# Optimization experiments

Measured on AMD Instinct MI355X. Metric: run time of the kernel, lower is better.

The kernel has to match this reference:

```python
import jax, jax.numpy as jnp
import numpy as np

N_NODES = 100000
N_EDGES = 1600000
DIM = 128
NUM_CLASSES = 40


def setup_inputs() -> dict:
    key = jax.random.key(0)
    ks = jax.random.split(key, 8)
    scale = 1.0 / np.sqrt(DIM)
    return {
        "node_embeddings": jax.random.normal(ks[0], (N_NODES, DIM), jnp.float32),
        "edge_index": jax.random.randint(ks[1], (N_EDGES, 2), 0, N_NODES, jnp.int32),
        "W1a": jax.random.normal(ks[2], (DIM, DIM), jnp.float32) * scale,
        "b1a": jnp.zeros((DIM,), jnp.float32),
        "W1b": jax.random.normal(ks[3], (DIM, DIM), jnp.float32) * scale,
        "b1b": jnp.zeros((DIM,), jnp.float32),
        "W2a": jax.random.normal(ks[4], (DIM, NUM_CLASSES), jnp.float32) * scale,
        "b2a": jnp.zeros((NUM_CLASSES,), jnp.float32),
        "W2b": jax.random.normal(ks[5], (NUM_CLASSES, NUM_CLASSES), jnp.float32) * (1.0 / np.sqrt(NUM_CLASSES)),
        "b2b": jnp.zeros((NUM_CLASSES,), jnp.float32),
    }


def _gin_conv(x, src, dst, Wa, ba, Wb, bb, n_nodes):
    # GIN aggregation with eps=0: h_i = (1+eps)*x_i + sum_{j in N(i)} x_j
    agg = jax.ops.segment_sum(x[src], dst, num_segments=n_nodes)
    h = agg + x
    # nn: Dense -> ReLU -> Dense
    h = jax.nn.relu(h @ Wa + ba)
    return h @ Wb + bb


def reference(node_embeddings, edge_index, W1a, b1a, W1b, b1b, W2a, b2a, W2b, b2b):
    src = edge_index[:, 0]
    dst = edge_index[:, 1]
    n = node_embeddings.shape[0]
    # dropout layers are identity at inference (predict: training=False)
    x = jax.nn.relu(_gin_conv(node_embeddings, src, dst, W1a, b1a, W1b, b1b, n))
    x = _gin_conv(x, src, dst, W2a, b2a, W2b, b2b, n)
    return jax.nn.softmax(x, axis=-1)
```

## Files before the change

kernel.cpp:

```cpp
#include <hip/hip_runtime.h>
#include <hip/hip_fp16.h>

#define N_NODES 100000
#define N_EDGES 1600000
#define DIM 128
#define NC 40

#define BUCKET_SHIFT 7
#define BUCKET_NODES 128
#define NBUCKET ((N_NODES + BUCKET_NODES - 1) / BUCKET_NODES)
#define SEGCAP 3072
#define NBIN 1024
#define EPB 4096
#define NBLK_FILL ((N_EDGES + EPB - 1) / EPB)

#define NBLK_CVT (N_NODES * DIM / 8 / 256)
#define NBLK_PACK 20

typedef _Float16 f16x8 __attribute__((ext_vector_type(8)));
typedef float f32x4 __attribute__((ext_vector_type(4)));

__device__ __forceinline__ void acc_row8(float* acc, uint4 v) {
    __half2 h;
    float2 f;
    *(unsigned*)&h = v.x; f = __half22float2(h); acc[0] += f.x; acc[1] += f.y;
    *(unsigned*)&h = v.y; f = __half22float2(h); acc[2] += f.x; acc[3] += f.y;
    *(unsigned*)&h = v.z; f = __half22float2(h); acc[4] += f.x; acc[5] += f.y;
    *(unsigned*)&h = v.w; f = __half22float2(h); acc[6] += f.x; acc[7] += f.y;
}

__global__ __launch_bounds__(256) void k_cvt_pack(const float* __restrict__ x, __half* __restrict__ xh,
                                                  __half* __restrict__ y,
                                                  const float* __restrict__ W1a, const float* __restrict__ W1b,
                                                  const float* __restrict__ W2a, const float* __restrict__ W2b,
                                                  _Float16* __restrict__ Pa, _Float16* __restrict__ Pb,
                                                  _Float16* __restrict__ Pc, float4* __restrict__ Wq) {
    int b = blockIdx.x, tid = threadIdx.x;
    if (b >= NBLK_CVT) {
        int bid = b - NBLK_CVT;
        if (bid < 16) {
            const float* W = (bid < 8) ? W1a : W1b;
            _Float16* P = (bid < 8) ? Pa : Pb;
            int t = (bid & 7) * 256 + tid;
            int l = t & 63, nt = (t >> 6) & 7, kt = t >> 9;
            int n = nt * 16 + (l & 15);
            int kb = kt * 32 + (l >> 4) * 8;
            #pragma unroll
            for (int j = 0; j < 8; ++j)
                P[(size_t)t * 8 + j] = (_Float16)W[(size_t)(kb + j) * DIM + n];
        } else if (bid < 19) {
            int t = (bid - 16) * 256 + tid;
            if (t < 768) {
                int l = t & 63, u = t >> 6;
                int nt = u % 3, kt = u / 3;
                int n = nt * 16 + (l & 15);
                int kb = kt * 32 + (l >> 4) * 8;
                #pragma unroll
                for (int j = 0; j < 8; ++j) {
                    float wv = (n < NC) ? W2a[(size_t)(kb + j) * NC + n] : 0.f;
                    Pc[(size_t)t * 8 + j] = (_Float16)wv;
                }
            }
        } else {
            for (int u = tid; u < 10 * NC; u += 256) {
                int q = u / NC, c = u - q * NC;
                float4 wv;
                wv.x = W2b[(4 * q + 0) * NC + c];
                wv.y = W2b[(4 * q + 1) * NC + c];
                wv.z = W2b[(4 * q + 2) * NC + c];
                wv.w = W2b[(4 * q + 3) * NC + c];
                Wq[u] = wv;
            }
        }
        return;
    }

    int i = b * 256 + tid;
    if (b == 0) {
        if (tid < 16) ((uint4*)xh)[(size_t)N_NODES * (DIM / 8) + tid] = (uint4){0, 0, 0, 0};
        else if (tid < 21) ((uint4*)y)[(size_t)N_NODES * 5 + tid - 16] = (uint4){0, 0, 0, 0};
    }
    float4 v0 = ((const float4*)x)[(size_t)i * 2];
    float4 v1 = ((const float4*)x)[(size_t)i * 2 + 1];
    __half2 h01 = __float22half2_rn(make_float2(v0.x, v0.y));
    __half2 h23 = __float22half2_rn(make_float2(v0.z, v0.w));
    __half2 h45 = __float22half2_rn(make_float2(v1.x, v1.y));
    __half2 h67 = __float22half2_rn(make_float2(v1.z, v1.w));
    uint4 o;
    o.x = *(unsigned*)&h01; o.y = *(unsigned*)&h23;
    o.z = *(unsigned*)&h45; o.w = *(unsigned*)&h67;
    ((uint4*)xh)[i] = o;
}

__global__ __launch_bounds__(256) void k_binfill(const int2* __restrict__ ei, int* __restrict__ cnt,
                                                 int* __restrict__ seg) {
    __shared__ int hist[NBIN];
    __shared__ int offs[NBIN];
    __shared__ int gbase[NBIN];
    __shared__ int lcnt[NBIN];
    __shared__ int lds[EPB];
    __shared__ short binof[EPB];
    __shared__ int wt[4];
    int t = threadIdx.x;
    int e0 = blockIdx.x * EPB;
    int bec = N_EDGES - e0; if (bec > EPB) bec = EPB;

    int2 er[EPB / 256];
    #pragma unroll
    for (int k = 0; k < EPB / 256; ++k) {
        int i = e0 + t + k * 256;
        er[k] = (i < N_EDGES) ? ei[i] : (int2){0, -1};
    }

    #pragma unroll
    for (int j = 0; j < NBIN / 256; ++j) { hist[t + j * 256] = 0; lcnt[t + j * 256] = 0; }
    __syncthreads();

    #pragma unroll
    for (int k = 0; k < EPB / 256; ++k)
        if (er[k].y >= 0) atomicAdd(&hist[er[k].y >> BUCKET_SHIFT], 1);
    __syncthreads();

    int lane = t & 63, w = t >> 6;
    int h[4], p = 0;
    #pragma unroll
    for (int j = 0; j < 4; ++j) { h[j] = hist[t * 4 + j]; p += h[j]; }
    int inc = p;
    #pragma unroll
    for (int d = 1; d < 64; d <<= 1) {
        int u = __shfl_up(inc, d, 64);
        if (lane >= d) inc += u;
    }
    if (lane == 63) wt[w] = inc;
    __syncthreads();
    int add = inc - p;
    for (int k = 0; k < w; ++k) add += wt[k];
    int run = add;
    #pragma unroll
    for (int j = 0; j < 4; ++j) { offs[t * 4 + j] = run; run += h[j]; }
    __syncthreads();

    #pragma unroll
    for (int j = 0; j < 4; ++j) {
        int b = t * 4 + j;
        if (b < NBUCKET && h[j] > 0) gbase[b] = b * SEGCAP + atomicAdd(&cnt[b], h[j]);
    }
    __syncthreads();

    #pragma unroll
    for (int k = 0; k < EPB / 256; ++k) {
        if (er[k].y >= 0) {
            int b = er[k].y >> BUCKET_SHIFT;
            int pos = offs[b] + atomicAdd(&lcnt[b], 1);
            lds[pos] = er[k].x | ((er[k].y & (BUCKET_NODES - 1)) << 17);
            binof[pos] = (short)b;
        }
    }
    __syncthreads();

    for (int i = t; i < bec; i += 256) {
        int lo = binof[i];
        seg[gbase[lo] + (i - offs[lo])] = lds[i];
    }
}

__global__ __launch_bounds__(256) void k_csr_local(int* __restrict__ dg, const int* __restrict__ cnt,
                                                   const int* __restrict__ seg, int* __restrict__ rs,
                                                   int* __restrict__ csr) {
    __shared__ int ldg[BUCKET_NODES];
    __shared__ int cur[BUCKET_NODES];
    __shared__ int wq0;
    int t = threadIdx.x, b = blockIdx.x;
    int n0 = b * BUCKET_NODES;
    int nn = N_NODES - n0; if (nn > BUCKET_NODES) nn = BUCKET_NODES;
    if (t < BUCKET_NODES) ldg[t] = 0;
    __syncthreads();

    int c = cnt[b];
    for (int i = t; i < c; i += 256)
        atomicAdd(&ldg[(seg[b * SEGCAP + i] >> 17) & (BUCKET_NODES - 1)], 1);
    __syncthreads();

    int d = (t < BUCKET_NODES) ? ldg[t] : 0;
    int lane = t & 63, w2 = t >> 6;
    int incl = d;
    #pragma unroll
    for (int s = 1; s < 64; s <<= 1) {
        int u = __shfl_up(incl, s, 64);
        if (lane >= s) incl += u;
    }
    if (w2 == 0 && lane == 63) wq0 = incl;
    __syncthreads();
    int excl = incl - d + ((w2 == 1) ? wq0 : 0);
    if (t < nn) {
        int base = b * SEGCAP + excl;
        cur[t] = base;
        rs[n0 + t] = base;
        dg[n0 + t] = d;
    }
    __syncthreads();

    for (int i = t; i < c; i += 256) {
        int e = seg[b * SEGCAP + i];
        int dl = (e >> 17) & (BUCKET_NODES - 1);
        int pos = atomicAdd(&cur[dl], 1);
        csr[pos] = e & 0x1FFFF;
    }
}

__global__ __launch_bounds__(256) void k_gather1(const __half* __restrict__ xh, const int* __restrict__ rs,
                                                 const int* __restrict__ dg, const int* __restrict__ csr_src,
                                                 __half* __restrict__ hp) {
    int l = threadIdx.x & 63, wid = threadIdx.x >> 6;
    int n = __builtin_amdgcn_readfirstlane(blockIdx.x * 4 + wid);
    int grp = l >> 4, q = l & 15;
    const uint4* x4 = (const uint4*)xh;

    uint4 sv;
    if (grp == 0) sv = x4[(size_t)n * 16 + q];

    float acc[8] = {0.f, 0.f, 0.f, 0.f, 0.f, 0.f, 0.f, 0.f};
    int i0 = rs[n], e = i0 + dg[n];
    int niter = (e - i0 + 7) >> 3;
    uint4 cur[2];
    if (niter > 0) {
        #pragma unroll
        for (int u = 0; u < 2; ++u) {
            int idx = i0 + u * 4 + grp;
            int s = (idx < e) ? csr_src[idx] : N_NODES;
            cur[u] = x4[(size_t)s * 16 + q];
        }
    }
    for (int k = 1; k < niter; ++k) {
        int base = i0 + k * 8;
        uint4 nxt[2];
        #pragma unroll
        for (int u = 0; u < 2; ++u) {
            int idx = base + u * 4 + grp;
            int s = (idx < e) ? csr_src[idx] : N_NODES;
            nxt[u] = x4[(size_t)s * 16 + q];
        }
        acc_row8(acc, cur[0]); cur[0] = nxt[0];
        acc_row8(acc, cur[1]); cur[1] = nxt[1];
    }
    if (niter > 0) {
        acc_row8(acc, cur[0]);
        acc_row8(acc, cur[1]);
    }
    #pragma unroll
    for (int k2 = 0; k2 < 8; ++k2) {
        acc[k2] += __shfl_xor(acc[k2], 16);
        acc[k2] += __shfl_xor(acc[k2], 32);
    }

    if (grp == 0) {
        acc_row8(acc, sv);
        __half2 o0 = __float22half2_rn(make_float2(acc[0], acc[1]));
        __half2 o1 = __float22half2_rn(make_float2(acc[2], acc[3]));
        __half2 o2 = __float22half2_rn(make_float2(acc[4], acc[5]));
        __half2 o3 = __float22half2_rn(make_float2(acc[6], acc[7]));
        uint4 ov;
        ov.x = *(unsigned*)&o0; ov.y = *(unsigned*)&o1;
        ov.z = *(unsigned*)&o2; ov.w = *(unsigned*)&o3;
        ((uint4*)hp)[(size_t)n * 16 + q] = ov;
    }
}

__global__ __launch_bounds__(256) void k_mlp(const __half* __restrict__ hp,
    const _Float16* __restrict__ Pa, const _Float16* __restrict__ Pb, const _Float16* __restrict__ Pc,
    const float* __restrict__ b1a, const float* __restrict__ b1b, __half* __restrict__ y) {
    __shared__ _Float16 A[64][136];
    __shared__ _Float16 H[64][136];
    int t = threadIdx.x;
    size_t row0 = (size_t)blockIdx.x * 64;

    for (int i = t; i < 1024; i += 256) {
        int r = i >> 4, c = i & 15;
        size_t g = row0 + r;
        if (g >= N_NODES) g = N_NODES - 1;
        uint4 v = ((const uint4*)(hp + g * DIM))[c];
        *(uint4*)&A[r][c * 8] = v;
    }
    __syncthreads();

    int w = t >> 6, l = t & 63;
    int lrow = l & 15;
    int kq = (l >> 4) * 8;
    int csub = (l >> 4) * 4;
    int ccol = l & 15;
    int nt0 = 2 * w, nt1 = 2 * w + 1;

    {
        f16x8 bf0[4], bf1[4];
        #pragma unroll
        for (int kt = 0; kt < 4; ++kt) {
            bf0[kt] = *(const f16x8*)(Pa + ((size_t)((kt << 3) + nt0) * 64 + l) * 8);
            bf1[kt] = *(const f16x8*)(Pa + ((size_t)((kt << 3) + nt1) * 64 + l) * 8);
        }
        float b0 = b1a[nt0 * 16 + ccol], b1 = b1a[nt1 * 16 + ccol];
        #pragma unroll
        for (int rt = 0; rt < 4; ++rt) {
            f16x8 af[4];
            #pragma unroll
            for (int kt = 0; kt < 4; ++kt) af[kt] = *(const f16x8*)&A[rt * 16 + lrow][kt * 32 + kq];
            f32x4 a0 = (f32x4){b0, b0, b0, b0}, a1 = (f32x4){b1, b1, b1, b1};
            #pragma unroll
            for (int kt = 0; kt < 4; ++kt) {
                a0 = __builtin_amdgcn_mfma_f32_16x16x32_f16(af[kt], bf0[kt], a0, 0, 0, 0);
                a1 = __builtin_amdgcn_mfma_f32_16x16x32_f16(af[kt], bf1[kt], a1, 0, 0, 0);
            }
            #pragma unroll
            for (int r = 0; r < 4; ++r) {
                H[rt * 16 + csub + r][nt0 * 16 + ccol] = (_Float16)fmaxf(a0[r], 0.f);
                H[rt * 16 + csub + r][nt1 * 16 + ccol] = (_Float16)fmaxf(a1[r], 0.f);
            }
        }
    }
    __syncthreads();

    {
        f16x8 bf0[4], bf1[4];
        #pragma unroll
        for (int kt = 0; kt < 4; ++kt) {
            bf0[kt] = *(const f16x8*)(Pb + ((size_t)((kt << 3) + nt0) * 64 + l) * 8);
            bf1[kt] = *(const f16x8*)(Pb + ((size_t)((kt << 3) + nt1) * 64 + l) * 8);
        }
        float b0 = b1b[nt0 * 16 + ccol], b1 = b1b[nt1 * 16 + ccol];
        #pragma unroll
        for (int rt = 0; rt < 4; ++rt) {
            f16x8 af[4];
            #pragma unroll
            for (int kt = 0; kt < 4; ++kt) af[kt] = *(const f16x8*)&H[rt * 16 + lrow][kt * 32 + kq];
            f32x4 a0 = (f32x4){b0, b0, b0, b0}, a1 = (f32x4){b1, b1, b1, b1};
            #pragma unroll
            for (int kt = 0; kt < 4; ++kt) {
                a0 = __builtin_amdgcn_mfma_f32_16x16x32_f16(af[kt], bf0[kt], a0, 0, 0, 0);
                a1 = __builtin_amdgcn_mfma_f32_16x16x32_f16(af[kt], bf1[kt], a1, 0, 0, 0);
            }
            #pragma unroll
            for (int r = 0; r < 4; ++r) {
                A[rt * 16 + csub + r][nt0 * 16 + ccol] = (_Float16)fmaxf(a0[r], 0.f);
                A[rt * 16 + csub + r][nt1 * 16 + ccol] = (_Float16)fmaxf(a1[r], 0.f);
            }
        }
    }
    __syncthreads();

    #pragma unroll
    for (int it = 0; it < 3; ++it) {
        int tt = w + 4 * it;
        int nt = tt % 3, rt = tt / 3;
        f16x8 bf[4], af[4];
        #pragma unroll
        for (int kt = 0; kt < 4; ++kt) {
            bf[kt] = *(const f16x8*)(Pc + ((size_t)(kt * 3 + nt) * 64 + l) * 8);
            af[kt] = *(const f16x8*)&A[rt * 16 + lrow][kt * 32 + kq];
        }
        f32x4 ya = (f32x4){0.f, 0.f, 0.f, 0.f};
        #pragma unroll
        for (int kt = 0; kt < 4; ++kt)
            ya = __builtin_amdgcn_mfma_f32_16x16x32_f16(af[kt], bf[kt], ya, 0, 0, 0);
        int col = nt * 16 + ccol;
        if (col < NC) {
            #pragma unroll
            for (int r = 0; r < 4; ++r) {
                size_t gr = row0 + rt * 16 + csub + r;
                if (gr < N_NODES) y[gr * NC + col] = __float2half(ya[r]);
            }
        }
    }
}

__global__ __launch_bounds__(256) void k_gather2(const __half* __restrict__ y, const int* __restrict__ rs,
                                                 const int* __restrict__ dg, const int* __restrict__ csr_src,
                                                 const float* __restrict__ b2a, const float4* __restrict__ Wq,
                                                 const float* __restrict__ b2b, float* __restrict__ out) {
    __shared__ float h2s[4][NC];
    int l = threadIdx.x & 63, wid = threadIdx.x >> 6;
    int n = __builtin_amdgcn_readfirstlane(blockIdx.x * 4 + wid);
    int g = l / 5, j = l - g * 5;
    const uint4* y4 = (const uint4*)y;

    float acc[8] = {0.f, 0.f, 0.f, 0.f, 0.f, 0.f, 0.f, 0.f};
    uint4 self;
    if (l < 5) self = y4[(size_t)n * 5 + j];

    int i0 = rs[n], d = dg[n];
    int e = i0 + d;
    uint4 c0, c1;
    {
        int iA = i0 + g;
        int sA = (g < 12 && iA < e) ? csr_src[iA] : N_NODES;
        c0 = y4[(size_t)sA * 5 + j];
        int iB = i0 + 12 + g;
        int sB = (g < 12 && iB < e) ? csr_src[iB] : N_NODES;
        c1 = y4[(size_t)sB * 5 + j];
    }
    int niter = (d + 23) / 24;
    for (int k = 1; k < niter; ++k) {
        int base = i0 + k * 24;
        int iA = base + g;
        int sA = (g < 12 && iA < e) ? csr_src[iA] : N_NODES;
        uint4 n0 = y4[(size_t)sA * 5 + j];
        int iB = base + 12 + g;
        int sB = (g < 12 && iB < e) ? csr_src[iB] : N_NODES;
        uint4 n1 = y4[(size_t)sB * 5 + j];
        acc_row8(acc, c0); c0 = n0;
        acc_row8(acc, c1); c1 = n1;
    }
    if (d > 0) {
        acc_row8(acc, c0);
        acc_row8(acc, c1);
    }
    if (l < 5) acc_row8(acc, self);

    #pragma unroll
    for (int k = 0; k < 8; ++k) acc[k] += __shfl_down(acc[k], 30);
    #pragma unroll
    for (int k = 0; k < 8; ++k) acc[k] += __shfl_down(acc[k], 15);
    #pragma unroll
    for (int k = 0; k < 8; ++k) acc[k] += __shfl_down(acc[k], 5) + __shfl_down(acc[k], 10);

    if (l < 5) {
        float4 b0 = *(const float4*)(b2a + 8 * l);
        float4 b1 = *(const float4*)(b2a + 8 * l + 4);
        float4 h0, h1;
        h0.x = fmaxf(acc[0] + b0.x, 0.f); h0.y = fmaxf(acc[1] + b0.y, 0.f);
        h0.z = fmaxf(acc[2] + b0.z, 0.f); h0.w = fmaxf(acc[3] + b0.w, 0.f);
        h1.x = fmaxf(acc[4] + b1.x, 0.f); h1.y = fmaxf(acc[5] + b1.y, 0.f);
        h1.z = fmaxf(acc[6] + b1.z, 0.f); h1.w = fmaxf(acc[7] + b1.w, 0.f);
        *(float4*)&h2s[wid][8 * l] = h0;
        *(float4*)&h2s[wid][8 * l + 4] = h1;
    }
    __threadfence_block();

    float logit = -__builtin_inff();
    if (l < NC) {
        float4 a4 = {0.f, 0.f, 0.f, 0.f};
        #pragma unroll
        for (int q = 0; q < 10; ++q) {
            float4 h4 = *(const float4*)&h2s[wid][4 * q];
            float4 w4 = Wq[q * NC + l];
            a4.x = fmaf(h4.x, w4.x, a4.x);
            a4.y = fmaf(h4.y, w4.y, a4.y);
            a4.z = fmaf(h4.z, w4.z, a4.z);
            a4.w = fmaf(h4.w, w4.w, a4.w);
        }
        logit = (a4.x + a4.y) + (a4.z + a4.w) + b2b[l];
    }
    float m = logit;
    #pragma unroll
    for (int d2 = 32; d2 >= 1; d2 >>= 1) m = fmaxf(m, __shfl_xor(m, d2, 64));
    float ev = (l < NC) ? __expf(logit - m) : 0.f;
    float s = ev;
    #pragma unroll
    for (int d2 = 32; d2 >= 1; d2 >>= 1) s += __shfl_xor(s, d2, 64);
    if (l < NC) out[(size_t)n * NC + l] = ev / s;
}

extern "C" void kernel_launch(void* const* d_in, const int* in_sizes, int n_in,
                              void* d_out, int out_size, void* d_ws, size_t ws_size,
                              hipStream_t stream) {
    const float* x   = (const float*)d_in[0];
    const int2*  ei  = (const int2*)d_in[1];
    const float* W1a = (const float*)d_in[2];
    const float* b1a = (const float*)d_in[3];
    const float* W1b = (const float*)d_in[4];
    const float* b1b = (const float*)d_in[5];
    const float* W2a = (const float*)d_in[6];
    const float* b2a = (const float*)d_in[7];
    const float* W2b = (const float*)d_in[8];
    const float* b2b = (const float*)d_in[9];
    float* out = (float*)d_out;

    char* w = (char*)d_ws;
    int*    dg     = (int*)(w + 0);
    int*    cnt    = (int*)(w + 400000);
    int*    rs     = (int*)(w + 403200);
    int*    csr    = (int*)(w + 803200);
    __half* xh     = (__half*)(w + 10412416);
    __half* hp     = (__half*)(w + 36012672);
    __half* y      = (__half*)(w + 61612672);
    _Float16* Pa   = (_Float16*)(w + 69612800);
    _Float16* Pb   = (_Float16*)(w + 69645568);
    _Float16* Pc   = (_Float16*)(w + 69678336);
    float4*   Wq   = (float4*)(w + 69690624);
    int*    seg    = (int*)hp;

    (void)hipMemsetAsync(w + 400000, 0, 3200, stream);
    k_cvt_pack <<<NBLK_CVT + NBLK_PACK, 256, 0, stream>>>(x, xh, y,
                                                          W1a, W1b, W2a, W2b, Pa, Pb, Pc, Wq);
    k_binfill  <<<NBLK_FILL, 256, 0, stream>>>(ei, cnt, seg);
    k_csr_local<<<NBUCKET, 256, 0, stream>>>(dg, cnt, seg, rs, csr);
    k_gather1  <<<N_NODES / 4, 256, 0, stream>>>(xh, rs, dg, csr, hp);
    k_mlp      <<<(N_NODES + 63) / 64, 256, 0, stream>>>(hp, Pa, Pb, Pc, b1a, b1b, y);
    k_gather2  <<<N_NODES / 4, 256, 0, stream>>>(y, rs, dg, csr, b2a, Wq, b2b, out);
}
```

Baseline: 300.7 us.

## Merge conversion/packing into CSR kernel and use LDS atomics for gather2 reduction

The fp32-to-fp16 conversion and weight packing move out of their own launch and into the CSR-building kernel as extra blocks, which removes one kernel launch and lets the two independent jobs run concurrently. In gather2, the shuffle-based cross-lane reduction and bias/ReLU step are replaced by float atomicAdds into a bias-initialised shared row, followed by an in-place ReLU. The atomics may contend on the same LDS addresses and make the summation order nondeterministic. The ordering between the bias write and the atomics relies only on __threadfence_block within a wave.

```diff
diff --git a/kernel.cpp b/kernel.cpp
--- a/kernel.cpp
+++ b/kernel.cpp
@@ -27,69 +27,6 @@
     *(unsigned*)&h = v.y; f = __half22float2(h); acc[2] += f.x; acc[3] += f.y;
     *(unsigned*)&h = v.z; f = __half22float2(h); acc[4] += f.x; acc[5] += f.y;
     *(unsigned*)&h = v.w; f = __half22float2(h); acc[6] += f.x; acc[7] += f.y;
-}
-
-__global__ __launch_bounds__(256) void k_cvt_pack(const float* __restrict__ x, __half* __restrict__ xh,
-                                                  __half* __restrict__ y,
-                                                  const float* __restrict__ W1a, const float* __restrict__ W1b,
-                                                  const float* __restrict__ W2a, const float* __restrict__ W2b,
-                                                  _Float16* __restrict__ Pa, _Float16* __restrict__ Pb,
-                                                  _Float16* __restrict__ Pc, float4* __restrict__ Wq) {
-    int b = blockIdx.x, tid = threadIdx.x;
-    if (b >= NBLK_CVT) {
-        int bid = b - NBLK_CVT;
-        if (bid < 16) {
-            const float* W = (bid < 8) ? W1a : W1b;
-            _Float16* P = (bid < 8) ? Pa : Pb;
-            int t = (bid & 7) * 256 + tid;
-            int l = t & 63, nt = (t >> 6) & 7, kt = t >> 9;
-            int n = nt * 16 + (l & 15);
-            int kb = kt * 32 + (l >> 4) * 8;
-            #pragma unroll
-            for (int j = 0; j < 8; ++j)
-                P[(size_t)t * 8 + j] = (_Float16)W[(size_t)(kb + j) * DIM + n];
-        } else if (bid < 19) {
-            int t = (bid - 16) * 256 + tid;
-            if (t < 768) {
-                int l = t & 63, u = t >> 6;
-                int nt = u % 3, kt = u / 3;
-                int n = nt * 16 + (l & 15);
-                int kb = kt * 32 + (l >> 4) * 8;
-                #pragma unroll
-                for (int j = 0; j < 8; ++j) {
-                    float wv = (n < NC) ? W2a[(size_t)(kb + j) * NC + n] : 0.f;
-                    Pc[(size_t)t * 8 + j] = (_Float16)wv;
-                }
-            }
-        } else {
-            for (int u = tid; u < 10 * NC; u += 256) {
-                int q = u / NC, c = u - q * NC;
-                float4 wv;
-                wv.x = W2b[(4 * q + 0) * NC + c];
-                wv.y = W2b[(4 * q + 1) * NC + c];
-                wv.z = W2b[(4 * q + 2) * NC + c];
-                wv.w = W2b[(4 * q + 3) * NC + c];
-                Wq[u] = wv;
-            }
-        }
-        return;
-    }
-
-    int i = b * 256 + tid;
-    if (b == 0) {
-        if (tid < 16) ((uint4*)xh)[(size_t)N_NODES * (DIM / 8) + tid] = (uint4){0, 0, 0, 0};
-        else if (tid < 21) ((uint4*)y)[(size_t)N_NODES * 5 + tid - 16] = (uint4){0, 0, 0, 0};
-    }
-    float4 v0 = ((const float4*)x)[(size_t)i * 2];
-    float4 v1 = ((const float4*)x)[(size_t)i * 2 + 1];
-    __half2 h01 = __float22half2_rn(make_float2(v0.x, v0.y));
-    __half2 h23 = __float22half2_rn(make_float2(v0.z, v0.w));
-    __half2 h45 = __float22half2_rn(make_float2(v1.x, v1.y));
-    __half2 h67 = __float22half2_rn(make_float2(v1.z, v1.w));
-    uint4 o;
-    o.x = *(unsigned*)&h01; o.y = *(unsigned*)&h23;
-    o.z = *(unsigned*)&h45; o.w = *(unsigned*)&h67;
-    ((uint4*)xh)[i] = o;
 }
 
 __global__ __launch_bounds__(256) void k_binfill(const int2* __restrict__ ei, int* __restrict__ cnt,
@@ -164,47 +101,113 @@
     }
 }
 
-__global__ __launch_bounds__(256) void k_csr_local(int* __restrict__ dg, const int* __restrict__ cnt,
-                                                   const int* __restrict__ seg, int* __restrict__ rs,
-                                                   int* __restrict__ csr) {
+__global__ __launch_bounds__(256) void k_mid(int* __restrict__ dg, const int* __restrict__ cnt,
+                                             const int* __restrict__ seg, int* __restrict__ rs,
+                                             int* __restrict__ csr,
+                                             const float* __restrict__ x, __half* __restrict__ xh,
+                                             __half* __restrict__ y,
+                                             const float* __restrict__ W1a, const float* __restrict__ W1b,
+                                             const float* __restrict__ W2a, const float* __restrict__ W2b,
+                                             _Float16* __restrict__ Pa, _Float16* __restrict__ Pb,
+                                             _Float16* __restrict__ Pc, float4* __restrict__ Wq) {
     __shared__ int ldg[BUCKET_NODES];
     __shared__ int cur[BUCKET_NODES];
     __shared__ int wq0;
-    int t = threadIdx.x, b = blockIdx.x;
-    int n0 = b * BUCKET_NODES;
-    int nn = N_NODES - n0; if (nn > BUCKET_NODES) nn = BUCKET_NODES;
-    if (t < BUCKET_NODES) ldg[t] = 0;
-    __syncthreads();
-
-    int c = cnt[b];
-    for (int i = t; i < c; i += 256)
-        atomicAdd(&ldg[(seg[b * SEGCAP + i] >> 17) & (BUCKET_NODES - 1)], 1);
-    __syncthreads();
-
-    int d = (t < BUCKET_NODES) ? ldg[t] : 0;
-    int lane = t & 63, w2 = t >> 6;
-    int incl = d;
-    #pragma unroll
-    for (int s = 1; s < 64; s <<= 1) {
-        int u = __shfl_up(incl, s, 64);
-        if (lane >= s) incl += u;
-    }
-    if (w2 == 0 && lane == 63) wq0 = incl;
-    __syncthreads();
-    int excl = incl - d + ((w2 == 1) ? wq0 : 0);
-    if (t < nn) {
-        int base = b * SEGCAP + excl;
-        cur[t] = base;
-        rs[n0 + t] = base;
-        dg[n0 + t] = d;
-    }
-    __syncthreads();
-
-    for (int i = t; i < c; i += 256) {
-        int e = seg[b * SEGCAP + i];
-        int dl = (e >> 17) & (BUCKET_NODES - 1);
-        int pos = atomicAdd(&cur[dl], 1);
-        csr[pos] = e & 0x1FFFF;
+    int b = blockIdx.x, t = threadIdx.x;
+
+    if (b < NBUCKET) {
+        int n0 = b * BUCKET_NODES;
+        int nn = N_NODES - n0; if (nn > BUCKET_NODES) nn = BUCKET_NODES;
+        if (t < BUCKET_NODES) ldg[t] = 0;
+        __syncthreads();
+
+        int c = cnt[b];
+        for (int i = t; i < c; i += 256)
+            atomicAdd(&ldg[(seg[b * SEGCAP + i] >> 17) & (BUCKET_NODES - 1)], 1);
+        __syncthreads();
+
+        int d = (t < BUCKET_NODES) ? ldg[t] : 0;
+        int lane = t & 63, w2 = t >> 6;
+        int incl = d;
+        #pragma unroll
+        for (int s = 1; s < 64; s <<= 1) {
+            int u = __shfl_up(incl, s, 64);
+            if (lane >= s) incl += u;
+        }
+        if (w2 == 0 && lane == 63) wq0 = incl;
+        __syncthreads();
+        int excl = incl - d + ((w2 == 1) ? wq0 : 0);
+        if (t < nn) {
+            int base = b * SEGCAP + excl;
+            cur[t] = base;
+            rs[n0 + t] = base;
+            dg[n0 + t] = d;
+        }
+        __syncthreads();
+
+        for (int i = t; i < c; i += 256) {
+            int e = seg[b * SEGCAP + i];
+            int dl = (e >> 17) & (BUCKET_NODES - 1);
+            int pos = atomicAdd(&cur[dl], 1);
+            csr[pos] = e & 0x1FFFF;
+        }
+        return;
+    }
+
+    int cb = b - NBUCKET;
+    if (cb < NBLK_CVT) {
+        int i = cb * 256 + t;
+        if (cb == 0) {
+            if (t < 16) ((uint4*)xh)[(size_t)N_NODES * (DIM / 8) + t] = (uint4){0, 0, 0, 0};
+            else if (t < 21) ((uint4*)y)[(size_t)N_NODES * 5 + t - 16] = (uint4){0, 0, 0, 0};
+        }
+        float4 v0 = ((const float4*)x)[(size_t)i * 2];
+        float4 v1 = ((const float4*)x)[(size_t)i * 2 + 1];
+        __half2 h01 = __float22half2_rn(make_float2(v0.x, v0.y));
+        __half2 h23 = __float22half2_rn(make_float2(v0.z, v0.w));
+        __half2 h45 = __float22half2_rn(make_float2(v1.x, v1.y));
+        __half2 h67 = __float22half2_rn(make_float2(v1.z, v1.w));
+        uint4 o;
+        o.x = *(unsigned*)&h01; o.y = *(unsigned*)&h23;
+        o.z = *(unsigned*)&h45; o.w = *(unsigned*)&h67;
+        ((uint4*)xh)[i] = o;
+        return;
+    }
+
+    int bid = cb - NBLK_CVT;
+    if (bid < 16) {
+        const float* W = (bid < 8) ? W1a : W1b;
+        _Float16* P = (bid < 8) ? Pa : Pb;
+        int tt = (bid & 7) * 256 + t;
+        int l = tt & 63, nt = (tt >> 6) & 7, kt = tt >> 9;
+        int n = nt * 16 + (l & 15);
+        int kb = kt * 32 + (l >> 4) * 8;
+        #pragma unroll
+        for (int j = 0; j < 8; ++j)
+            P[(size_t)tt * 8 + j] = (_Float16)W[(size_t)(kb + j) * DIM + n];
+    } else if (bid < 19) {
+        int tt = (bid - 16) * 256 + t;
+        if (tt < 768) {
+            int l = tt & 63, u = tt >> 6;
+            int nt = u % 3, kt = u / 3;
+            int n = nt * 16 + (l & 15);
+            int kb = kt * 32 + (l >> 4) * 8;
+            #pragma unroll
+            for (int j = 0; j < 8; ++j) {
+                float wv = (n < NC) ? W2a[(size_t)(kb + j) * NC + n] : 0.f;
+                Pc[(size_t)tt * 8 + j] = (_Float16)wv;
+            }
+        }
+    } else {
+        for (int u = t; u < 10 * NC; u += 256) {
+            int q = u / NC, c = u - q * NC;
+            float4 wv;
+            wv.x = W2b[(4 * q + 0) * NC + c];
+            wv.y = W2b[(4 * q + 1) * NC + c];
+            wv.z = W2b[(4 * q + 2) * NC + c];
+            wv.w = W2b[(4 * q + 3) * NC + c];
+            Wq[u] = wv;
+        }
     }
 }
 
@@ -384,6 +387,8 @@
     float acc[8] = {0.f, 0.f, 0.f, 0.f, 0.f, 0.f, 0.f, 0.f};
     uint4 self;
     if (l < 5) self = y4[(size_t)n * 5 + j];
+
+    if (l < NC) h2s[wid][l] = b2a[l];
 
     int i0 = rs[n], d = dg[n];
     int e = i0 + d;
@@ -414,24 +419,13 @@
     }
     if (l < 5) acc_row8(acc, self);
 
-    #pragma unroll
-    for (int k = 0; k < 8; ++k) acc[k] += __shfl_down(acc[k], 30);
-    #pragma unroll
-    for (int k = 0; k < 8; ++k) acc[k] += __shfl_down(acc[k], 15);
-    #pragma unroll
-    for (int k = 0; k < 8; ++k) acc[k] += __shfl_down(acc[k], 5) + __shfl_down(acc[k], 10);
-
-    if (l < 5) {
-        float4 b0 = *(const float4*)(b2a + 8 * l);
-        float4 b1 = *(const float4*)(b2a + 8 * l + 4);
-        float4 h0, h1;
-        h0.x = fmaxf(acc[0] + b0.x, 0.f); h0.y = fmaxf(acc[1] + b0.y, 0.f);
-        h0.z = fmaxf(acc[2] + b0.z, 0.f); h0.w = fmaxf(acc[3] + b0.w, 0.f);
-        h1.x = fmaxf(acc[4] + b1.x, 0.f); h1.y = fmaxf(acc[5] + b1.y, 0.f);
-        h1.z = fmaxf(acc[6] + b1.z, 0.f); h1.w = fmaxf(acc[7] + b1.w, 0.f);
-        *(float4*)&h2s[wid][8 * l] = h0;
-        *(float4*)&h2s[wid][8 * l + 4] = h1;
-    }
+    __threadfence_block();
+    if (l < 60) {
+        #pragma unroll
+        for (int k = 0; k < 8; ++k) atomicAdd(&h2s[wid][j * 8 + k], acc[k]);
+    }
+    __threadfence_block();
+    if (l < NC) h2s[wid][l] = fmaxf(h2s[wid][l], 0.f);
     __threadfence_block();
 
     float logit = -__builtin_inff();
@@ -488,10 +482,10 @@
     int*    seg    = (int*)hp;
 
     (void)hipMemsetAsync(w + 400000, 0, 3200, stream);
-    k_cvt_pack <<<NBLK_CVT + NBLK_PACK, 256, 0, stream>>>(x, xh, y,
-                                                          W1a, W1b, W2a, W2b, Pa, Pb, Pc, Wq);
     k_binfill  <<<NBLK_FILL, 256, 0, stream>>>(ei, cnt, seg);
-    k_csr_local<<<NBUCKET, 256, 0, stream>>>(dg, cnt, seg, rs, csr);
+    k_mid      <<<NBUCKET + NBLK_CVT + NBLK_PACK, 256, 0, stream>>>(dg, cnt, seg, rs, csr,
+                                                                    x, xh, y, W1a, W1b, W2a, W2b,
+                                                                    Pa, Pb, Pc, Wq);
     k_gather1  <<<N_NODES / 4, 256, 0, stream>>>(xh, rs, dg, csr, hp);
     k_mlp      <<<(N_NODES + 63) / 64, 256, 0, stream>>>(hp, Pa, Pb, Pc, b1a, b1b, y);
     k_gather2  <<<N_NODES / 4, 256, 0, stream>>>(y, rs, dg, csr, b2a, Wq, b2b, out);
```

Result: slower. 500.2 us (+66.4%).
